# Kernel optimization log

Measured on AMD Instinct MI355X. Metric: run time of the kernel, lower is better.

The kernel has to match this reference:

```python
import jax, jax.numpy as jnp
import numpy as np

B, N, D, EPG = 64, 1024, 128, 8192          # graphs, nodes/graph, feat dim, edges/graph
NTOT, ETOT = B * N, B * EPG
RATIO, LAMB, NEG = 0.8, 1.0, 0.2
K = int(np.ceil(RATIO * N))                  # 820 kept nodes per graph (static)


def setup_inputs() -> dict:
    key = jax.random.key(0)
    k1, k2, k3, k4, k5, k6 = jax.random.split(key, 6)
    feat = jax.random.normal(k1, (NTOT, D), jnp.float32)
    offs = (jnp.arange(B, dtype=jnp.int32) * N)[:, None]
    src = (jax.random.randint(k2, (B, EPG), 0, N, jnp.int32) + offs).reshape(-1)
    dst = (jax.random.randint(k3, (B, EPG), 0, N, jnp.int32) + offs).reshape(-1)
    e_feat = jnp.ones((ETOT,), jnp.float32)  # default e_feat=None -> ones
    # xavier-normal-ish params
    W = jax.random.normal(k4, (D, D), jnp.float32) * (2.0 / (D + D)) ** 0.5
    a = jax.random.normal(k5, (D, 1), jnp.float32) * (2.0 / (D + 1)) ** 0.5
    att = jax.random.normal(k6, (1, 2 * D), jnp.float32) * (2.0 / (1 + 2 * D)) ** 0.5
    return {"feat": feat, "e_feat": e_feat, "W": W, "a": a, "att": att,
            "src": src, "dst": dst}


def sparsemax(z, axis):
    """Dense sparsemax along `axis` (shift-invariant, same as edge_sparsemax
    per destination-node group after max subtraction)."""
    n = z.shape[axis]
    zs = -jnp.sort(-z, axis=axis)                      # descending
    cs = jnp.cumsum(zs, axis=axis)
    shp = [1] * z.ndim
    shp[axis] = n
    r = jnp.arange(1, n + 1, dtype=z.dtype).reshape(shp)
    supp = (1.0 + r * zs) > cs
    kz = supp.sum(axis=axis, keepdims=True)            # support size
    tau = (jnp.take_along_axis(cs, kz - 1, axis=axis) - 1.0) / kz.astype(z.dtype)
    return jnp.clip(z - tau, 0.0)


def reference(feat, e_feat, W, a, att, src, dst):
    # ---- NodeInfoScoreLayer (sym_norm=True) ----
    ones_e = jnp.ones_like(e_feat)
    out_deg = jax.ops.segment_sum(ones_e, src, NTOT)   # degrees incl. self loops
    in_deg = jax.ops.segment_sum(ones_e, dst, NTOT)
    sn = jnp.maximum(out_deg, 1.0) ** -0.5
    dn = jnp.maximum(in_deg, 1.0) ** -0.5
    nonself = (src != dst).astype(feat.dtype)          # remove_self_loop
    msg = (feat * sn[:, None])[src] * (e_feat * nonself)[:, None]   # u_mul_e
    agg = jax.ops.segment_sum(msg, dst, NTOT)                        # sum -> h
    info = jnp.abs(feat - agg * dn[:, None]).sum(axis=1)

    # ---- node attention gate ----
    attn = jax.nn.sigmoid(jax.nn.leaky_relu((feat @ W) @ a, 0.2).squeeze(-1))
    x_score = info * attn

    # ---- per-graph top-k (equal graph sizes -> static k) ----
    _, idx = jax.lax.top_k(x_score.reshape(B, N), K)
    perm = (idx + jnp.arange(B, dtype=idx.dtype)[:, None] * N).reshape(-1)
    feat_p = feat[perm]                                # [B*K, D]

    # ---- structure learning, sample=False path: per-graph dense blocks ----
    maskarr = jnp.full((NTOT,), -1, jnp.int32).at[perm].set(
        jnp.arange(B * K, dtype=jnp.int32))
    nr, nc = maskarr[src], maskarr[dst]
    valid = (nr >= 0) & (nc >= 0)                      # edges of pooled subgraph
    nr0 = jnp.where(valid, nr, 0)
    nc0 = jnp.where(valid, nc, 0)
    bb, ii, jj = nr0 // K, nr0 % K, nc0 % K            # block-diagonal coords

    fp = feat_p.reshape(B, K, D)
    wsrc = fp @ att[0, :D]                             # [B, K]
    wdst = fp @ att[0, D:]
    Wblk = jax.nn.leaky_relu(wsrc[:, :, None] + wdst[:, None, :], NEG)  # [B,K,K]
    Wblk = Wblk.at[bb, ii, jj].add(jnp.where(valid, LAMB * e_feat, 0.0))

    # edge_sparsemax: normalize over incoming edges of each dst node
    weights = sparsemax(Wblk, axis=1)                  # over src axis
    weights = jnp.where(jnp.abs(weights) > 1e-9, weights, 0.0)

    return feat_p, weights, perm, x_score
```

## Files before the change

### kernel.cpp

```cpp
#include <hip/hip_runtime.h>
#include <math.h>


static constexpr int B_    = 64;
static constexpr int N_    = 1024;
static constexpr int D_    = 128;
static constexpr int NTOT_ = B_ * N_;
static constexpr int ETOT_ = B_ * 8192;
static constexpr int K_    = 820;
static constexpr int BK_   = B_ * K_;
static constexpr float NEG_ = 0.2f;
static constexpr int CH_   = 128;
static constexpr int CPB_  = 7;
static constexpr int CAP_  = 64;

__device__ __forceinline__ float lrelu(float x) { return x >= 0.f ? x : NEG_ * x; }

__global__ void k_wa(const float* __restrict__ W, const float* __restrict__ a,
                     float* __restrict__ waf) {
  int d = threadIdx.x;
  double s = 0.0;
  for (int k = 0; k < D_; ++k) s += (double)W[d * D_ + k] * (double)a[k];
  waf[d] = (float)s;
}

__global__ void k_deg(const int* __restrict__ src, const int* __restrict__ dst,
                      int* __restrict__ outd, int* __restrict__ ind) {
  int e = blockIdx.x * 256 + threadIdx.x;
  atomicAdd(&outd[src[e]], 1);
  atomicAdd(&ind[dst[e]], 1);
}

__global__ void k_scansum(const int* __restrict__ in, int n, int* __restrict__ bsum) {
  int blk = blockIdx.x, t = threadIdx.x;
  int base = blk * 1024 + t * 4;
  int s = 0;
#pragma unroll
  for (int q = 0; q < 4; ++q) { int i = base + q; if (i < n) s += in[i]; }
#pragma unroll
  for (int off = 32; off > 0; off >>= 1) s += __shfl_down(s, off);
  __shared__ int ws[4];
  int w = t >> 6, lane = t & 63;
  if (lane == 0) ws[w] = s;
  __syncthreads();
  if (t == 0) bsum[blk] = ws[0] + ws[1] + ws[2] + ws[3];
}

__global__ void k_scanout(const int* __restrict__ in, int n,
                          const int* __restrict__ bsum, int* __restrict__ out) {
  int blk = blockIdx.x, t = threadIdx.x;
  int w = t >> 6, lane = t & 63;
  __shared__ int sbase;
  __shared__ int wtot[4];
  if (w == 0) {
    int v = (lane < blk) ? bsum[lane] : 0;
#pragma unroll
    for (int off = 32; off > 0; off >>= 1) v += __shfl_down(v, off);
    if (lane == 0) sbase = v;
  }
  int base = blk * 1024 + t * 4;
  int a0 = (base < n) ? in[base] : 0;
  int a1 = (base + 1 < n) ? in[base + 1] : 0;
  int a2 = (base + 2 < n) ? in[base + 2] : 0;
  int a3 = (base + 3 < n) ? in[base + 3] : 0;
  int s = a0 + a1 + a2 + a3;
  int inc = s;
#pragma unroll
  for (int off = 1; off < 64; off <<= 1) {
    int vv = __shfl_up(inc, off);
    if (lane >= off) inc += vv;
  }
  if (lane == 63) wtot[w] = inc;
  __syncthreads();
  int wbase = 0;
  for (int q = 0; q < w; ++q) wbase += wtot[q];
  int ex = sbase + wbase + inc - s;
  if (base < n) out[base] = ex; ex += a0;
  if (base + 1 < n) out[base + 1] = ex; ex += a1;
  if (base + 2 < n) out[base + 2] = ex; ex += a2;
  if (base + 3 < n) out[base + 3] = ex; ex += a3;
  if (blk == (int)gridDim.x - 1 && t == 255) out[n] = ex;
}

__global__ void k_fillcsr(const int* __restrict__ dst, const int* __restrict__ rowptr,
                          int* __restrict__ cursor, int* __restrict__ col) {
  int e = blockIdx.x * 256 + threadIdx.x;
  int v = dst[e];
  int p = atomicAdd(&cursor[v], 1);
  col[rowptr[v] + p] = e;
}

__global__ void k_agg(const float* __restrict__ feat, const float* __restrict__ e_feat,
                      const int* __restrict__ src, const int* __restrict__ col,
                      const int* __restrict__ rowptr, const int* __restrict__ outd,
                      const int* __restrict__ ind, const float* __restrict__ waf,
                      float* __restrict__ out_xs) {
  __shared__ int su[4][CAP_];
  __shared__ float ssc[4][CAP_];
  int g = blockIdx.x;
  int vb = (g & 7) * 2048 + (g >> 3);
  int w = threadIdx.x >> 6, lane = threadIdx.x & 63;
  int v = vb * 4 + w;
  int r0 = rowptr[v], r1 = rowptr[v + 1];
  int m = r1 - r0;
  int mm = m < CAP_ ? m : CAP_;
  for (int s = lane; s < mm; s += 64) {
    int e = col[r0 + s];
    int u = src[e];
    float sc = (u == v) ? 0.f : e_feat[e] / sqrtf(fmaxf((float)outd[u], 1.f));
    su[w][s] = u;
    ssc[w][s] = sc;
  }
  __syncthreads();
  const float2* f2 = (const float2*)feat;
  float2 f = f2[(size_t)v * 64 + lane];
  float ax = 0.f, ay = 0.f;
  int s = 0;
  for (; s + 4 <= mm; s += 4) {
    int u0 = su[w][s], u1 = su[w][s + 1], u2 = su[w][s + 2], u3 = su[w][s + 3];
    float c0 = ssc[w][s], c1 = ssc[w][s + 1], c2 = ssc[w][s + 2], c3 = ssc[w][s + 3];
    float2 f0 = f2[(size_t)u0 * 64 + lane];
    float2 f1 = f2[(size_t)u1 * 64 + lane];
    float2 fq = f2[(size_t)u2 * 64 + lane];
    float2 f3 = f2[(size_t)u3 * 64 + lane];
    ax += f0.x * c0 + f1.x * c1 + fq.x * c2 + f3.x * c3;
    ay += f0.y * c0 + f1.y * c1 + fq.y * c2 + f3.y * c3;
  }
  for (; s < mm; ++s) {
    float2 fu = f2[(size_t)su[w][s] * 64 + lane];
    ax += fu.x * ssc[w][s];
    ay += fu.y * ssc[w][s];
  }
  for (int sP = r0 + CAP_; sP < r1; ++sP) {
    int e = col[sP];
    int u = src[e];
    if (u == v) continue;
    float sc = e_feat[e] / sqrtf(fmaxf((float)outd[u], 1.f));
    float2 fu = f2[(size_t)u * 64 + lane];
    ax += fu.x * sc;
    ay += fu.y * sc;
  }
  float dn = 1.f / sqrtf(fmaxf((float)ind[v], 1.f));
  float info = fabsf(f.x - ax * dn) + fabsf(f.y - ay * dn);
  float dot = f.x * waf[2 * lane] + f.y * waf[2 * lane + 1];
#pragma unroll
  for (int off = 32; off > 0; off >>= 1) {
    info += __shfl_down(info, off);
    dot  += __shfl_down(dot, off);
  }
  if (lane == 0) {
    float sA = dot >= 0.f ? dot : 0.2f * dot;
    float attn = 1.f / (1.f + expf(-sA));
    out_xs[v] = info * attn;
  }
}

__global__ void k_topk(const float* __restrict__ xs, float* __restrict__ out_perm,
                       int* __restrict__ perm_i, int* __restrict__ maskarr) {
  __shared__ unsigned long long dv[1024];
  int b = blockIdx.x, t = threadIdx.x;
  for (int i = t; i < 1024; i += 512) {
    unsigned bits = __float_as_uint(xs[b * 1024 + i]);
    dv[i] = ((unsigned long long)bits << 32) | (unsigned)(N_ - 1 - i);
  }
  __syncthreads();
  for (int k2 = 2; k2 <= 1024; k2 <<= 1) {
    for (int j = k2 >> 1; j > 0; j >>= 1) {
      for (int i = t; i < 1024; i += 512) {
        int ixj = i ^ j;
        if (ixj > i) {
          unsigned long long a = dv[i], c = dv[ixj];
          bool dir = ((i & k2) == 0);
          if ((a > c) != dir) { dv[i] = c; dv[ixj] = a; }
        }
      }
      __syncthreads();
    }
  }
  for (int r = t; r < K_; r += 512) {
    int idx = N_ - 1 - (int)(dv[r] & 0xFFFFFFFFull);
    int node = b * N_ + idx;
    int pos = b * K_ + r;
    out_perm[pos] = (float)node;
    perm_i[pos] = node;
    maskarr[node] = pos;
  }
}

__global__ void k_gather(const float* __restrict__ feat, const int* __restrict__ perm_i,
                         const float* __restrict__ att, float* __restrict__ out_featp,
                         float* __restrict__ wsrc, float* __restrict__ wdst) {
  int g = blockIdx.x;
  int vb = (g & 7) * 1640 + (g >> 3);
  int gid = vb * 256 + threadIdx.x;
  int p = gid >> 6, lane = gid & 63;
  int node = perm_i[p];
  float2 f = ((const float2*)feat)[(size_t)node * 64 + lane];
  ((float2*)out_featp)[(size_t)p * 64 + lane] = f;
  float s1 = f.x * att[2 * lane] + f.y * att[2 * lane + 1];
  float s2 = f.x * att[D_ + 2 * lane] + f.y * att[D_ + 2 * lane + 1];
#pragma unroll
  for (int off = 32; off > 0; off >>= 1) {
    s1 += __shfl_down(s1, off);
    s2 += __shfl_down(s2, off);
  }
  if (lane == 0) { wsrc[p] = s1; wdst[p] = s2; }
}

__global__ void k_cnt2(const int* __restrict__ src, const int* __restrict__ dst,
                       const int* __restrict__ maskarr, int* __restrict__ cnt2) {
  int e = blockIdx.x * 256 + threadIdx.x;
  int nr = maskarr[src[e]], nc = maskarr[dst[e]];
  if (nr >= 0 && nc >= 0) atomicAdd(&cnt2[nc], 1);
}

__global__ void k_fill2(const int* __restrict__ src, const int* __restrict__ dst,
                        const int* __restrict__ maskarr, const float* __restrict__ e_feat,
                        const int* __restrict__ rowptr2, int* __restrict__ cursor2,
                        int* __restrict__ colii, float* __restrict__ colval) {
  int e = blockIdx.x * 256 + threadIdx.x;
  int nr = maskarr[src[e]], nc = maskarr[dst[e]];
  if (nr >= 0 && nc >= 0) {
    int p = atomicAdd(&cursor2[nc], 1);
    int s = rowptr2[nc] + p;
    colii[s] = nr;
    colval[s] = 1.0f * e_feat[e];
  }
}

__global__ void k_dedupe(const int* __restrict__ rowptr2, int* __restrict__ colii,
                         float* __restrict__ colval, int* __restrict__ ucnt,
                         const float* __restrict__ wsrc, float2* __restrict__ bval) {
  int c = blockIdx.x * 256 + threadIdx.x;
  int r0 = rowptr2[c], r1 = rowptr2[c + 1];
  int w = r0;
  for (int s = r0; s < r1; ++s) {
    int ii = colii[s];
    if (ii < 0) continue;
    float E = colval[s];
    for (int t2 = s + 1; t2 < r1; ++t2)
      if (colii[t2] == ii) { E += colval[t2]; colii[t2] = -1; }
    colii[w] = ii; colval[w] = E; ++w;
  }
  ucnt[c] = w - r0;
  for (int s = r0; s < w; ++s) bval[s] = make_float2(wsrc[colii[s]], colval[s]);
}

__global__ void k_gsort(const float* __restrict__ wsrc, float* __restrict__ ws_sorted,
                        float* __restrict__ psum) {
  __shared__ float sv[1024];
  __shared__ float sc[1024];
  int b = blockIdx.x, t = threadIdx.x;
  for (int i = t; i < 1024; i += 512) sv[i] = (i < K_) ? wsrc[b * K_ + i] : -INFINITY;
  __syncthreads();
  for (int k2 = 2; k2 <= 1024; k2 <<= 1) {
    for (int j = k2 >> 1; j > 0; j >>= 1) {
      for (int i = t; i < 1024; i += 512) {
        int ixj = i ^ j;
        if (ixj > i) {
          float a = sv[i], c = sv[ixj];
          bool dir = ((i & k2) == 0);
          bool swapv = dir ? (c > a) : (a > c);
          if (swapv) { sv[i] = c; sv[ixj] = a; }
        }
      }
      __syncthreads();
    }
  }
  for (int i = t; i < 1024; i += 512) { ws_sorted[b * 1024 + i] = sv[i]; sc[i] = sv[i]; }
  __syncthreads();
  for (int off = 1; off < 1024; off <<= 1) {
    float tmp[2];
    for (int i = t, q = 0; i < 1024; i += 512, ++q) tmp[q] = (i >= off) ? sc[i - off] : 0.f;
    __syncthreads();
    for (int i = t, q = 0; i < 1024; i += 512, ++q) sc[i] += tmp[q];
    __syncthreads();
  }
  if (t == 0) psum[b * 1025] = 0.f;
  for (int i = t; i < 1024; i += 512) psum[b * 1025 + 1 + i] = sc[i];
}

__device__ __forceinline__ int cnt_gt_rng(const float* __restrict__ arr, float thr,
                                          int lo, int hi) {
  while (lo < hi) {
    int mid = (lo + hi) >> 1;
    if (arr[mid] > thr) lo = mid + 1; else hi = mid;
  }
  return lo;
}

__global__ void __launch_bounds__(128) k_tau(
    const float* __restrict__ wdst,
    const float* __restrict__ ws_sorted, const float* __restrict__ psum,
    const int* __restrict__ rowptr2, const int* __restrict__ ucnt,
    const float2* __restrict__ bval, float* __restrict__ tauv) {
  __shared__ float swss[1024];
  __shared__ float sps[1025];
  int b = blockIdx.x / CPB_;
  int chunk = blockIdx.x % CPB_;
  int t0 = threadIdx.x;
  for (int i = t0; i < 1024; i += 128) swss[i] = ws_sorted[b * 1024 + i];
  for (int i = t0; i < 1025; i += 128) sps[i] = psum[b * 1025 + i];
  __syncthreads();

  int j = chunk * CH_ + t0;
  if (j >= K_) return;
  int c = b * K_ + j;

  float wd = wdst[c];
  int p = cnt_gt_rng(swss, -wd, 0, K_);
  float psp = sps[p];
  int r0 = rowptr2[c], m = ucnt[c];

  float mz = lrelu(swss[0] + wd);
  for (int s = 0; s < m; ++s) {
    float2 v = bval[r0 + s];
    mz = fmaxf(mz, lrelu(v.x + wd) + v.y);
  }

  float lo = mz - 1.0f, hi = mz;
  int nmin = 0, nmax = K_;
  for (int it = 0; it < 22; ++it) {
    float t = 0.5f * (lo + hi);
    float wthr = (t >= 0.f ? t : 5.f * t) - wd;
    int n = cnt_gt_rng(swss, wthr, nmin, nmax);
    float bsum = (n <= p) ? (sps[n] + n * wd)
                          : (psp + p * wd + NEG_ * (sps[n] - psp + (n - p) * wd));
    float g = bsum - n * t;
    for (int s = 0; s < m; ++s) {
      float2 v = bval[r0 + s];
      float bse = lrelu(v.x + wd);
      g += fmaxf(bse + v.y - t, 0.f) - fmaxf(bse - t, 0.f);
    }
    if (g > 1.f) { lo = t; nmax = n; } else { hi = t; nmin = n; }
  }
  float t = lo;
  float wthr = (t >= 0.f ? t : 5.f * t) - wd;
  int n = cnt_gt_rng(swss, wthr, nmin, nmax);
  float S = (n <= p) ? (sps[n] + n * wd)
                     : (psp + p * wd + NEG_ * (sps[n] - psp + (n - p) * wd));
  int cc = n;
  for (int s = 0; s < m; ++s) {
    float2 v = bval[r0 + s];
    float bse = lrelu(v.x + wd);
    float zz = bse + v.y;
    if (v.x > wthr) { S -= bse; cc -= 1; }
    if (zz > t)     { S += zz;  cc += 1; }
  }
  float tau = (cc < 1) ? (mz - 1.0f) : ((S - 1.0f) / (float)cc);
  tau = fminf(fmaxf(tau, mz - 1.0f), mz);
  tauv[c] = tau;
}

__global__ void k_dense(const float* __restrict__ wsrc, const float* __restrict__ wdst,
                        const float* __restrict__ tauv, float* __restrict__ out_w) {
  int t = threadIdx.x;
  int j4 = t * 4;
  if (j4 >= K_) return;
  int row = blockIdx.x;
  int b = row / K_;
  const float4* wd4 = (const float4*)(wdst + b * K_);
  const float4* ta4 = (const float4*)(tauv + b * K_);
  float ws = wsrc[row];
  float4 wd = wd4[t];
  float4 ta = ta4[t];
  float4 o;
  float z;
  z = lrelu(ws + wd.x) - ta.x; o.x = (z > 1e-9f) ? z : 0.f;
  z = lrelu(ws + wd.y) - ta.y; o.y = (z > 1e-9f) ? z : 0.f;
  z = lrelu(ws + wd.z) - ta.z; o.z = (z > 1e-9f) ? z : 0.f;
  z = lrelu(ws + wd.w) - ta.w; o.w = (z > 1e-9f) ? z : 0.f;
  ((float4*)(out_w + (size_t)row * K_))[t] = o;
}

__global__ void k_fix(const float* __restrict__ wsrc, const float* __restrict__ wdst,
                      const float* __restrict__ tauv, const int* __restrict__ rowptr2,
                      const int* __restrict__ ucnt, const int* __restrict__ colii,
                      const float* __restrict__ colval, float* __restrict__ out_w) {
  int c = blockIdx.x * 256 + threadIdx.x;
  int b = c / K_;
  int j = c - b * K_;
  float wd = wdst[c], ta = tauv[c];
  int r0 = rowptr2[c], m = ucnt[c];
  for (int s = 0; s < m; ++s) {
    int nr = colii[r0 + s];
    float z = lrelu(wsrc[nr] + wd) + colval[r0 + s];
    float v = z - ta;
    out_w[(size_t)nr * K_ + j] = (v > 1e-9f) ? v : 0.f;
  }
}

extern "C" void kernel_launch(void* const* d_in, const int* in_sizes, int n_in,
                              void* d_out, int out_size, void* d_ws, size_t ws_size,
                              hipStream_t stream) {
  const float* feat   = (const float*)d_in[0];
  const float* e_feat = (const float*)d_in[1];
  const float* W      = (const float*)d_in[2];
  const float* a      = (const float*)d_in[3];
  const float* att    = (const float*)d_in[4];
  const int*   src    = (const int*)d_in[5];
  const int*   dst    = (const int*)d_in[6];

  float* out_featp = (float*)d_out;
  float* out_w     = out_featp + (size_t)BK_ * D_;
  float* out_perm  = out_w + (size_t)BK_ * K_;
  float* out_xs    = out_perm + BK_;

  char* wsp = (char*)d_ws;
  auto carve = [&](size_t bytes) -> void* {
    void* pp = (void*)wsp;
    wsp += (bytes + 255) & ~(size_t)255;
    return pp;
  };
  float* waf       = (float*)carve((size_t)D_ * 4);
  float* wsrc      = (float*)carve((size_t)BK_ * 4);
  float* wdst      = (float*)carve((size_t)BK_ * 4);
  float* tauv      = (float*)carve((size_t)BK_ * 4);
  float* colval    = (float*)carve((size_t)ETOT_ * 4);
  float2* bval     = (float2*)carve((size_t)ETOT_ * 8);
  float* ws_sorted = (float*)carve((size_t)B_ * 1024 * 4);
  float* psum      = (float*)carve((size_t)B_ * 1025 * 4);
  int* rowptr      = (int*)carve((size_t)(NTOT_ + 1) * 4);
  int* rowptr2     = (int*)carve((size_t)(BK_ + 1) * 4);
  int* col         = (int*)carve((size_t)ETOT_ * 4);
  int* colii       = (int*)carve((size_t)ETOT_ * 4);
  int* perm_i      = (int*)carve((size_t)BK_ * 4);
  int* bsumA       = (int*)carve(64 * 4);
  int* bsumB       = (int*)carve(64 * 4);
  size_t zbytes    = ((size_t)NTOT_ * 3 + (size_t)BK_ * 2) * 4;
  int* zblk        = (int*)carve(zbytes);
  int* in_deg      = zblk;
  int* out_deg     = zblk + NTOT_;
  int* cursor      = zblk + 2 * NTOT_;
  int* cnt2        = zblk + 3 * NTOT_;
  int* cursor2     = cnt2 + BK_;
  int* maskarr     = (int*)carve((size_t)NTOT_ * 4);

  hipMemsetAsync(zblk, 0, zbytes, stream);
  hipMemsetAsync(maskarr, 0xFF, (size_t)NTOT_ * 4, stream);

  const int nbA = (NTOT_ + 1023) / 1024;
  const int nbB = (BK_ + 1023) / 1024;

  k_wa<<<1, 128, 0, stream>>>(W, a, waf);
  k_deg<<<ETOT_ / 256, 256, 0, stream>>>(src, dst, out_deg, in_deg);
  k_scansum<<<nbA, 256, 0, stream>>>(in_deg, NTOT_, bsumA);
  k_scanout<<<nbA, 256, 0, stream>>>(in_deg, NTOT_, bsumA, rowptr);
  k_fillcsr<<<ETOT_ / 256, 256, 0, stream>>>(dst, rowptr, cursor, col);
  k_agg<<<NTOT_ / 4, 256, 0, stream>>>(feat, e_feat, src, col, rowptr, out_deg, in_deg,
                                       waf, out_xs);
  k_topk<<<B_, 512, 0, stream>>>(out_xs, out_perm, perm_i, maskarr);
  k_gather<<<BK_ / 4, 256, 0, stream>>>(feat, perm_i, att, out_featp, wsrc, wdst);
  k_cnt2<<<ETOT_ / 256, 256, 0, stream>>>(src, dst, maskarr, cnt2);
  k_scansum<<<nbB, 256, 0, stream>>>(cnt2, BK_, bsumB);
  k_scanout<<<nbB, 256, 0, stream>>>(cnt2, BK_, bsumB, rowptr2);
  k_fill2<<<ETOT_ / 256, 256, 0, stream>>>(src, dst, maskarr, e_feat, rowptr2, cursor2,
                                           colii, colval);
  k_dedupe<<<BK_ / 256, 256, 0, stream>>>(rowptr2, colii, colval, cursor2, wsrc, bval);
  k_gsort<<<B_, 512, 0, stream>>>(wsrc, ws_sorted, psum);
  k_tau<<<B_ * CPB_, 128, 0, stream>>>(wdst, ws_sorted, psum, rowptr2, cursor2,
                                       bval, tauv);
  k_dense<<<BK_, 256, 0, stream>>>(wsrc, wdst, tauv, out_w);
  k_fix<<<BK_ / 256, 256, 0, stream>>>(wsrc, wdst, tauv, rowptr2, cursor2, colii, colval,
                                       out_w);
}
```

Measured before the change: 539.5 us.

## Fuse independent kernels to cut launches and widen agg gathers to float4

Merges several independent kernel pairs into single launches: weight-vector and degree counting, gather and pooled-edge counting, dedupe and per-graph sort. The two-kernel scan becomes one kernel in which each block re-reduces its whole prefix. The aggregation kernel now splits each wavefront into two half-waves that read float4 rows and handle alternating edges, then combines the halves with a shuffle. The aim is fewer launches and serial steps, in exchange for redundant prefix reads in the scan and mixed block roles that may unbalance the fused launches.

Measured after the change: 560.7 us. +3.9%, slower.

```diff
diff --git a/kernel.cpp b/kernel.cpp
--- a/kernel.cpp
+++ b/kernel.cpp
@@ -13,52 +13,41 @@
 static constexpr int CH_   = 128;
 static constexpr int CPB_  = 7;
 static constexpr int CAP_  = 64;
+static constexpr int NDED_ = (BK_ + 511) / 512;
 
 __device__ __forceinline__ float lrelu(float x) { return x >= 0.f ? x : NEG_ * x; }
 
-__global__ void k_wa(const float* __restrict__ W, const float* __restrict__ a,
-                     float* __restrict__ waf) {
-  int d = threadIdx.x;
-  double s = 0.0;
-  for (int k = 0; k < D_; ++k) s += (double)W[d * D_ + k] * (double)a[k];
-  waf[d] = (float)s;
-}
-
-__global__ void k_deg(const int* __restrict__ src, const int* __restrict__ dst,
-                      int* __restrict__ outd, int* __restrict__ ind) {
-  int e = blockIdx.x * 256 + threadIdx.x;
-  atomicAdd(&outd[src[e]], 1);
-  atomicAdd(&ind[dst[e]], 1);
-}
-
-__global__ void k_scansum(const int* __restrict__ in, int n, int* __restrict__ bsum) {
-  int blk = blockIdx.x, t = threadIdx.x;
-  int base = blk * 1024 + t * 4;
-  int s = 0;
-#pragma unroll
-  for (int q = 0; q < 4; ++q) { int i = base + q; if (i < n) s += in[i]; }
-#pragma unroll
-  for (int off = 32; off > 0; off >>= 1) s += __shfl_down(s, off);
-  __shared__ int ws[4];
-  int w = t >> 6, lane = t & 63;
-  if (lane == 0) ws[w] = s;
-  __syncthreads();
-  if (t == 0) bsum[blk] = ws[0] + ws[1] + ws[2] + ws[3];
-}
-
-__global__ void k_scanout(const int* __restrict__ in, int n,
-                          const int* __restrict__ bsum, int* __restrict__ out) {
+__global__ void k_wa_deg(const float* __restrict__ W, const float* __restrict__ a,
+                         float* __restrict__ waf, const int* __restrict__ src,
+                         const int* __restrict__ dst, int* __restrict__ outd,
+                         int* __restrict__ ind) {
+  int g = blockIdx.x, t = threadIdx.x;
+  if (g < 2048) {
+    int e = g * 256 + t;
+    atomicAdd(&outd[src[e]], 1);
+    atomicAdd(&ind[dst[e]], 1);
+  } else if (t < 128) {
+    double s = 0.0;
+    for (int k = 0; k < D_; ++k) s += (double)W[t * D_ + k] * (double)a[k];
+    waf[t] = (float)s;
+  }
+}
+
+__global__ void k_scan1(const int* __restrict__ in, int n, int* __restrict__ out) {
   int blk = blockIdx.x, t = threadIdx.x;
   int w = t >> 6, lane = t & 63;
   __shared__ int sbase;
+  __shared__ int wred[4];
   __shared__ int wtot[4];
-  if (w == 0) {
-    int v = (lane < blk) ? bsum[lane] : 0;
+  int pre = blk * 1024;
+  int s0 = 0;
+  for (int i = t; i < pre; i += 256) s0 += in[i];
 #pragma unroll
-    for (int off = 32; off > 0; off >>= 1) v += __shfl_down(v, off);
-    if (lane == 0) sbase = v;
-  }
-  int base = blk * 1024 + t * 4;
+  for (int off = 32; off > 0; off >>= 1) s0 += __shfl_down(s0, off);
+  if (lane == 0) wred[w] = s0;
+  __syncthreads();
+  if (t == 0) sbase = wred[0] + wred[1] + wred[2] + wred[3];
+  int base = pre + t * 4;
   int a0 = (base < n) ? in[base] : 0;
   int a1 = (base + 1 < n) ? in[base + 1] : 0;
   int a2 = (base + 2 < n) ? in[base + 2] : 0;
@@ -100,10 +89,12 @@
   int g = blockIdx.x;
   int vb = (g & 7) * 2048 + (g >> 3);
   int w = threadIdx.x >> 6, lane = threadIdx.x & 63;
+  int hd = lane >> 5, li = lane & 31;
   int v = vb * 4 + w;
   int r0 = rowptr[v], r1 = rowptr[v + 1];
   int m = r1 - r0;
   int mm = m < CAP_ ? m : CAP_;
+  for (int s = lane; s < CAP_; s += 64) { su[w][s] = 0; ssc[w][s] = 0.f; }
   for (int s = lane; s < mm; s += 64) {
     int e = col[r0 + s];
     int u = src[e];
@@ -112,41 +103,41 @@
     ssc[w][s] = sc;
   }
   __syncthreads();
-  const float2* f2 = (const float2*)feat;
-  float2 f = f2[(size_t)v * 64 + lane];
-  float ax = 0.f, ay = 0.f;
-  int s = 0;
-  for (; s + 4 <= mm; s += 4) {
-    int u0 = su[w][s], u1 = su[w][s + 1], u2 = su[w][s + 2], u3 = su[w][s + 3];
-    float c0 = ssc[w][s], c1 = ssc[w][s + 1], c2 = ssc[w][s + 2], c3 = ssc[w][s + 3];
-    float2 f0 = f2[(size_t)u0 * 64 + lane];
-    float2 f1 = f2[(size_t)u1 * 64 + lane];
-    float2 fq = f2[(size_t)u2 * 64 + lane];
-    float2 f3 = f2[(size_t)u3 * 64 + lane];
-    ax += f0.x * c0 + f1.x * c1 + fq.x * c2 + f3.x * c3;
-    ay += f0.y * c0 + f1.y * c1 + fq.y * c2 + f3.y * c3;
-  }
-  for (; s < mm; ++s) {
-    float2 fu = f2[(size_t)su[w][s] * 64 + lane];
-    ax += fu.x * ssc[w][s];
-    ay += fu.y * ssc[w][s];
+  const float4* f4 = (const float4*)feat;
+  float ax = 0.f, ay = 0.f, az = 0.f, aw = 0.f;
+  int mmp = (mm + 3) & ~3;
+  for (int s = 0; s < mmp; s += 4) {
+    int e0 = s + hd, e1 = s + 2 + hd;
+    int u0 = su[w][e0], u1 = su[w][e1];
+    float c0 = ssc[w][e0], c1 = ssc[w][e1];
+    float4 fa = f4[(size_t)u0 * 32 + li];
+    float4 fb = f4[(size_t)u1 * 32 + li];
+    ax += fa.x * c0 + fb.x * c1;
+    ay += fa.y * c0 + fb.y * c1;
+    az += fa.z * c0 + fb.z * c1;
+    aw += fa.w * c0 + fb.w * c1;
   }
   for (int sP = r0 + CAP_; sP < r1; ++sP) {
+    if (hd) break;
     int e = col[sP];
     int u = src[e];
     if (u == v) continue;
     float sc = e_feat[e] / sqrtf(fmaxf((float)outd[u], 1.f));
-    float2 fu = f2[(size_t)u * 64 + lane];
-    ax += fu.x * sc;
-    ay += fu.y * sc;
-  }
+    float4 fu = f4[(size_t)u * 32 + li];
+    ax += fu.x * sc; ay += fu.y * sc; az += fu.z * sc; aw += fu.w * sc;
+  }
+  ax += __shfl_xor(ax, 32); ay += __shfl_xor(ay, 32);
+  az += __shfl_xor(az, 32); aw += __shfl_xor(aw, 32);
+  float4 fv = f4[(size_t)v * 32 + li];
+  float4 wv = ((const float4*)waf)[li];
   float dn = 1.f / sqrtf(fmaxf((float)ind[v], 1.f));
-  float info = fabsf(f.x - ax * dn) + fabsf(f.y - ay * dn);
-  float dot = f.x * waf[2 * lane] + f.y * waf[2 * lane + 1];
+  float info = fabsf(fv.x - ax * dn) + fabsf(fv.y - ay * dn)
+             + fabsf(fv.z - az * dn) + fabsf(fv.w - aw * dn);
+  float dot = fv.x * wv.x + fv.y * wv.y + fv.z * wv.z + fv.w * wv.w;
 #pragma unroll
-  for (int off = 32; off > 0; off >>= 1) {
-    info += __shfl_down(info, off);
-    dot  += __shfl_down(dot, off);
+  for (int off = 16; off > 0; off >>= 1) {
+    info += __shfl_down(info, off, 32);
+    dot  += __shfl_down(dot, off, 32);
   }
   if (lane == 0) {
     float sA = dot >= 0.f ? dot : 0.2f * dot;
@@ -187,10 +178,20 @@
   }
 }
 
-__global__ void k_gather(const float* __restrict__ feat, const int* __restrict__ perm_i,
-                         const float* __restrict__ att, float* __restrict__ out_featp,
-                         float* __restrict__ wsrc, float* __restrict__ wdst) {
+__global__ void k_gather_cnt2(const float* __restrict__ feat,
+                              const int* __restrict__ perm_i,
+                              const float* __restrict__ att,
+                              float* __restrict__ out_featp,
+                              float* __restrict__ wsrc, float* __restrict__ wdst,
+                              const int* __restrict__ src, const int* __restrict__ dst,
+                              const int* __restrict__ maskarr, int* __restrict__ cnt2) {
   int g = blockIdx.x;
+  if (g >= 13120) {
+    int e = (g - 13120) * 256 + threadIdx.x;
+    int nr = maskarr[src[e]], nc = maskarr[dst[e]];
+    if (nr >= 0 && nc >= 0) atomicAdd(&cnt2[nc], 1);
+    return;
+  }
   int vb = (g & 7) * 1640 + (g >> 3);
   int gid = vb * 256 + threadIdx.x;
   int p = gid >> 6, lane = gid & 63;
@@ -207,13 +208,6 @@
   if (lane == 0) { wsrc[p] = s1; wdst[p] = s2; }
 }
 
-__global__ void k_cnt2(const int* __restrict__ src, const int* __restrict__ dst,
-                       const int* __restrict__ maskarr, int* __restrict__ cnt2) {
-  int e = blockIdx.x * 256 + threadIdx.x;
-  int nr = maskarr[src[e]], nc = maskarr[dst[e]];
-  if (nr >= 0 && nc >= 0) atomicAdd(&cnt2[nc], 1);
-}
-
 __global__ void k_fill2(const int* __restrict__ src, const int* __restrict__ dst,
                         const int* __restrict__ maskarr, const float* __restrict__ e_feat,
                         const int* __restrict__ rowptr2, int* __restrict__ cursor2,
@@ -228,29 +222,31 @@
   }
 }
 
-__global__ void k_dedupe(const int* __restrict__ rowptr2, int* __restrict__ colii,
-                         float* __restrict__ colval, int* __restrict__ ucnt,
-                         const float* __restrict__ wsrc, float2* __restrict__ bval) {
-  int c = blockIdx.x * 256 + threadIdx.x;
-  int r0 = rowptr2[c], r1 = rowptr2[c + 1];
-  int w = r0;
-  for (int s = r0; s < r1; ++s) {
-    int ii = colii[s];
-    if (ii < 0) continue;
-    float E = colval[s];
-    for (int t2 = s + 1; t2 < r1; ++t2)
-      if (colii[t2] == ii) { E += colval[t2]; colii[t2] = -1; }
-    colii[w] = ii; colval[w] = E; ++w;
-  }
-  ucnt[c] = w - r0;
-  for (int s = r0; s < w; ++s) bval[s] = make_float2(wsrc[colii[s]], colval[s]);
-}
-
-__global__ void k_gsort(const float* __restrict__ wsrc, float* __restrict__ ws_sorted,
-                        float* __restrict__ psum) {
+__global__ void k_ded_gsort(const int* __restrict__ rowptr2, int* __restrict__ colii,
+                            float* __restrict__ colval, int* __restrict__ ucnt,
+                            const float* __restrict__ wsrc, float2* __restrict__ bval,
+                            float* __restrict__ ws_sorted, float* __restrict__ psum) {
+  int g = blockIdx.x, t = threadIdx.x;
+  if (g < NDED_) {
+    int c = g * 512 + t;
+    if (c >= BK_) return;
+    int r0 = rowptr2[c], r1 = rowptr2[c + 1];
+    int w = r0;
+    for (int s = r0; s < r1; ++s) {
+      int ii = colii[s];
+      if (ii < 0) continue;
+      float E = colval[s];
+      for (int t2 = s + 1; t2 < r1; ++t2)
+        if (colii[t2] == ii) { E += colval[t2]; colii[t2] = -1; }
+      colii[w] = ii; colval[w] = E; ++w;
+    }
+    ucnt[c] = w - r0;
+    for (int s = r0; s < w; ++s) bval[s] = make_float2(wsrc[colii[s]], colval[s]);
+    return;
+  }
   __shared__ float sv[1024];
   __shared__ float sc[1024];
-  int b = blockIdx.x, t = threadIdx.x;
+  int b = g - NDED_;
   for (int i = t; i < 1024; i += 512) sv[i] = (i < K_) ? wsrc[b * K_ + i] : -INFINITY;
   __syncthreads();
   for (int k2 = 2; k2 <= 1024; k2 <<= 1) {
@@ -425,8 +421,6 @@
   int* col         = (int*)carve((size_t)ETOT_ * 4);
   int* colii       = (int*)carve((size_t)ETOT_ * 4);
   int* perm_i      = (int*)carve((size_t)BK_ * 4);
-  int* bsumA       = (int*)carve(64 * 4);
-  int* bsumB       = (int*)carve(64 * 4);
   size_t zbytes    = ((size_t)NTOT_ * 3 + (size_t)BK_ * 2) * 4;
   int* zblk        = (int*)carve(zbytes);
   int* in_deg      = zblk;
@@ -442,22 +436,19 @@
   const int nbA = (NTOT_ + 1023) / 1024;
   const int nbB = (BK_ + 1023) / 1024;
 
-  k_wa<<<1, 128, 0, stream>>>(W, a, waf);
-  k_deg<<<ETOT_ / 256, 256, 0, stream>>>(src, dst, out_deg, in_deg);
-  k_scansum<<<nbA, 256, 0, stream>>>(in_deg, NTOT_, bsumA);
-  k_scanout<<<nbA, 256, 0, stream>>>(in_deg, NTOT_, bsumA, rowptr);
+  k_wa_deg<<<2049, 256, 0, stream>>>(W, a, waf, src, dst, out_deg, in_deg);
+  k_scan1<<<nbA, 256, 0, stream>>>(in_deg, NTOT_, rowptr);
   k_fillcsr<<<ETOT_ / 256, 256, 0, stream>>>(dst, rowptr, cursor, col);
   k_agg<<<NTOT_ / 4, 256, 0, stream>>>(feat, e_feat, src, col, rowptr, out_deg, in_deg,
                                        waf, out_xs);
   k_topk<<<B_, 512, 0, stream>>>(out_xs, out_perm, perm_i, maskarr);
-  k_gather<<<BK_ / 4, 256, 0, stream>>>(feat, perm_i, att, out_featp, wsrc, wdst);
-  k_cnt2<<<ETOT_ / 256, 256, 0, stream>>>(src, dst, maskarr, cnt2);
-  k_scansum<<<nbB, 256, 0, stream>>>(cnt2, BK_, bsumB);
-  k_scanout<<<nbB, 256, 0, stream>>>(cnt2, BK_, bsumB, rowptr2);
+  k_gather_cnt2<<<13120 + 2048, 256, 0, stream>>>(feat, perm_i, att, out_featp,
+                                                  wsrc, wdst, src, dst, maskarr, cnt2);
+  k_scan1<<<nbB, 256, 0, stream>>>(cnt2, BK_, rowptr2);
   k_fill2<<<ETOT_ / 256, 256, 0, stream>>>(src, dst, maskarr, e_feat, rowptr2, cursor2,
                                            colii, colval);
-  k_dedupe<<<BK_ / 256, 256, 0, stream>>>(rowptr2, colii, colval, cursor2, wsrc, bval);
-  k_gsort<<<B_, 512, 0, stream>>>(wsrc, ws_sorted, psum);
+  k_ded_gsort<<<NDED_ + B_, 512, 0, stream>>>(rowptr2, colii, colval, cursor2, wsrc,
+                                              bval, ws_sorted, psum);
   k_tau<<<B_ * CPB_, 128, 0, stream>>>(wdst, ws_sorted, psum, rowptr2, cursor2,
                                        bval, tauv);
   k_dense<<<BK_, 256, 0, stream>>>(wsrc, wdst, tauv, out_w);
```
